# Optimization experiments

Measured on AMD Instinct MI355X. Metric: run time of the kernel, lower is better.

The kernel has to match this reference:

```python
import jax, jax.numpy as jnp
import numpy as np

D_MODEL, N_HEAD, D_HEAD = 1024, 16, 64
BATCH, Q_LEN = 2, 2048
LN_EPS = 1e-5


def _rel_shift(x):
    # x: [b, q, k, n] -- standard Transformer-XL relative shift
    b, q, k, n = x.shape
    zero_pad = jnp.zeros((b, q, 1, n), dtype=x.dtype)
    x_padded = jnp.concatenate([zero_pad, x], axis=2)      # [b, q, k+1, n]
    x_padded = x_padded.reshape(b, k + 1, q, n)
    return x_padded[:, 1:].reshape(b, q, k, n)


def _layer_norm(x, gamma, beta):
    mu = jnp.mean(x, axis=-1, keepdims=True)
    var = jnp.mean(jnp.square(x - mu), axis=-1, keepdims=True)
    return (x - mu) * jax.lax.rsqrt(var + LN_EPS) * gamma + beta


def setup_inputs() -> dict:
    key = jax.random.key(0)
    ks = jax.random.split(key, 8)
    inp = {
        "x": jax.random.normal(ks[0], (BATCH, Q_LEN, D_MODEL), jnp.float32),
        "relative_pos": jax.random.normal(ks[1], (Q_LEN, D_MODEL), jnp.float32),
        "r_w_bias": jax.random.normal(ks[2], (N_HEAD, D_HEAD), jnp.float32) * 0.02,
        "r_r_bias": jax.random.normal(ks[3], (N_HEAD, D_HEAD), jnp.float32) * 0.02,
        "attn_mask": jax.random.randint(ks[4], (BATCH, Q_LEN), 0, 2).astype(bool),
        "W_qkv": jax.random.normal(ks[5], (D_MODEL, 3 * N_HEAD * D_HEAD), jnp.float32) / np.sqrt(D_MODEL),
        "W_rel": jax.random.normal(ks[6], (D_MODEL, N_HEAD * D_HEAD), jnp.float32) / np.sqrt(D_MODEL),
        "W_out": jax.random.normal(ks[7], (N_HEAD * D_HEAD, D_MODEL), jnp.float32) / np.sqrt(N_HEAD * D_HEAD),
        "ln_gamma": jnp.ones((D_MODEL,), jnp.float32),
        "ln_beta": jnp.zeros((D_MODEL,), jnp.float32),
    }
    return inp


def reference(x, relative_pos, r_w_bias, r_r_bias, attn_mask, W_qkv, W_rel, W_out, ln_gamma, ln_beta):
    b, q_len, _ = x.shape
    r_len = relative_pos.shape[0]
    scale = 1.0 / np.sqrt(D_HEAD)

    w_heads = x @ W_qkv                                    # [b, q, 3*n*d]
    w_q, w_k, w_v = jnp.split(w_heads, 3, axis=-1)
    k_len = w_k.shape[1]

    w_q = w_q.reshape(b, q_len, N_HEAD, D_HEAD)
    w_k = w_k.reshape(b, k_len, N_HEAD, D_HEAD)
    w_v = w_v.reshape(b, k_len, N_HEAD, D_HEAD)
    r_k = (relative_pos @ W_rel).reshape(r_len, N_HEAD, D_HEAD)

    rw_q = w_q + r_w_bias                                  # [b, q, n, d]
    rr_q = w_q + r_r_bias

    ac = jnp.einsum('bind,bjnd->bijn', rw_q, w_k)          # content score
    bd = jnp.einsum('bind,jnd->bijn', rr_q, r_k)           # position score
    bd = _rel_shift(bd)

    attn_score = (ac + bd) * scale                         # [b, q, k, n]
    attn_score = jnp.where(attn_mask[:, None, :, None], -jnp.inf, attn_score)
    attn_prob = jax.nn.softmax(attn_score, axis=2)

    context = jnp.einsum('bijn,bjnd->bind', attn_prob, w_v)
    context = context.reshape(b, q_len, N_HEAD * D_HEAD)
    attn_out = context @ W_out
    return _layer_norm(x + attn_out, ln_gamma, ln_beta)
```

## Files before the change

### kernel.cpp

```cpp
#include <hip/hip_runtime.h>
#include <hip/hip_bf16.h>
#include <math.h>

#define S_LEN 2048
#define NHEAD 16
#define DHEAD 64
#define DMODEL 1024
#define NBATCH 2

typedef unsigned short u16;
typedef __attribute__((ext_vector_type(8))) short bf16x8;
typedef __attribute__((ext_vector_type(4))) short short4v;
typedef __attribute__((ext_vector_type(4))) float f32x4;

__device__ __forceinline__ short f2bs(float x) {
    __hip_bfloat16 h = __float2bfloat16(x);
    return __builtin_bit_cast(short, h);
}

#define GL2LDS(g, l)                                                         \
    __builtin_amdgcn_global_load_lds(                                        \
        (const __attribute__((address_space(1))) void*)(g),                  \
        (__attribute__((address_space(3))) void*)(l), 16, 0, 0)

__global__ __launch_bounds__(256) void cast_all(const float* __restrict__ x,
                                                const float* __restrict__ rpos,
                                                u16* __restrict__ xb,
                                                u16* __restrict__ rposb) {
    int bid = blockIdx.x;
    const float* in;
    u16* out;
    if (bid < 4096) { in = x; out = xb; }
    else            { in = rpos; out = rposb; bid -= 4096; }
    const int i = (bid * 256 + threadIdx.x) * 4;
    float4 v = *(const float4*)(in + i);
    short4v t;
    t[0] = f2bs(v.x); t[1] = f2bs(v.y); t[2] = f2bs(v.z); t[3] = f2bs(v.w);
    *(short4v*)(out + i) = t;
}

__global__ __launch_bounds__(256) void transp_cast_all(
    const float* __restrict__ Wqkv, const float* __restrict__ Wrel,
    const float* __restrict__ Wout,
    u16* __restrict__ Wqkvt, u16* __restrict__ Wrelt, u16* __restrict__ Woutt)
{
    __shared__ float t[64][65];
    int bx = blockIdx.x;
    const float* W;
    u16* Wt;
    int N;
    if (bx < 48)      { W = Wqkv; Wt = Wqkvt; N = 3 * DMODEL; }
    else if (bx < 64) { W = Wrel; Wt = Wrelt; N = DMODEL; bx -= 48; }
    else              { W = Wout; Wt = Woutt; N = DMODEL; bx -= 64; }
    const int k0 = blockIdx.y * 64, n0 = bx * 64;
    const int r = threadIdx.x >> 4;
    const int c4 = (threadIdx.x & 15) * 4;
    #pragma unroll
    for (int it = 0; it < 4; ++it) {
        float4 v = *(const float4*)(W + (size_t)(k0 + it * 16 + r) * N + n0 + c4);
        t[c4 + 0][it * 16 + r] = v.x;
        t[c4 + 1][it * 16 + r] = v.y;
        t[c4 + 2][it * 16 + r] = v.z;
        t[c4 + 3][it * 16 + r] = v.w;
    }
    __syncthreads();
    #pragma unroll
    for (int it = 0; it < 4; ++it) {
        const int nn = it * 16 + r;
        short4v o;
        o[0] = f2bs(t[nn][c4 + 0]); o[1] = f2bs(t[nn][c4 + 1]);
        o[2] = f2bs(t[nn][c4 + 2]); o[3] = f2bs(t[nn][c4 + 3]);
        *(short4v*)(Wt + (size_t)(n0 + nn) * DMODEL + k0 + c4) = o;
    }
}

#define GEMM_BODY(Aptr, Btptr, Kdim)                                          \
    __shared__ u16 As[128 * 64];                                              \
    __shared__ u16 Bs[128 * 64];                                              \
    const int tid = threadIdx.x;                                              \
    const int lane = tid & 63;                                                \
    const int w = tid >> 6;                                                   \
    const int quad = lane >> 4, col = lane & 15;                              \
    const int bm = blockIdx.y * 128, bn = blockIdx.x * 128;                   \
    const int wm = (w >> 1) * 64, wn = (w & 1) * 64;                          \
    f32x4 acc[4][4];                                                          \
    _Pragma("unroll")                                                         \
    for (int mt = 0; mt < 4; ++mt)                                            \
        _Pragma("unroll")                                                     \
        for (int nt = 0; nt < 4; ++nt) acc[mt][nt] = (f32x4){0.f,0.f,0.f,0.f};\
    for (int k0 = 0; k0 < (Kdim); k0 += 64) {                                 \
        _Pragma("unroll")                                                     \
        for (int it = 0; it < 4; ++it) {                                      \
            const int cb = it * 256 + w * 64;                                 \
            const int c = cb + lane;                                          \
            const int r = c >> 3;                                             \
            const int o = ((c & 7) ^ (r & 7)) * 8;                            \
            GL2LDS((Aptr) + (size_t)(bm + r) * (Kdim) + k0 + o, As + (size_t)cb * 8); \
            GL2LDS((Btptr) + (size_t)(bn + r) * (Kdim) + k0 + o, Bs + (size_t)cb * 8);\
        }                                                                     \
        __syncthreads();                                                      \
        _Pragma("unroll")                                                     \
        for (int kc = 0; kc < 2; ++kc) {                                      \
            bf16x8 af[4], bfr[4];                                             \
            _Pragma("unroll")                                                 \
            for (int t = 0; t < 4; ++t) {                                     \
                const int am = wm + t * 16 + col;                             \
                const int aj = kc * 4 + quad;                                 \
                af[t] = *(const bf16x8*)&As[(size_t)am * 64 + ((aj ^ (am & 7)) * 8)]; \
                const int bn2 = wn + t * 16 + col;                            \
                bfr[t] = *(const bf16x8*)&Bs[(size_t)bn2 * 64 + ((aj ^ (bn2 & 7)) * 8)]; \
            }                                                                 \
            _Pragma("unroll")                                                 \
            for (int mt = 0; mt < 4; ++mt)                                    \
                _Pragma("unroll")                                             \
                for (int nt = 0; nt < 4; ++nt)                                \
                    acc[mt][nt] = __builtin_amdgcn_mfma_f32_16x16x32_bf16(    \
                        af[mt], bfr[nt], acc[mt][nt], 0, 0, 0);               \
        }                                                                     \
        __syncthreads();                                                      \
    }

__global__ __launch_bounds__(256, 2) void gemm_qkv(
    const u16* __restrict__ A, const u16* __restrict__ Bt,
    const float* __restrict__ rwb, const float* __restrict__ rrb,
    u16* __restrict__ qrw_b, u16* __restrict__ qrr_b,
    u16* __restrict__ kb, u16* __restrict__ vbT)
{
    GEMM_BODY(A, Bt, DMODEL)
    #pragma unroll
    for (int mt = 0; mt < 4; ++mt) {
        const int row0 = bm + wm + mt * 16 + quad * 4;
        const int b = row0 >> 11;
        const int s0 = row0 & 2047;
        #pragma unroll
        for (int nt = 0; nt < 4; ++nt) {
            const int cn = bn + wn + nt * 16 + col;
            const int sec = cn >> 10;
            const int cc = cn & 1023;
            const int h = cc >> 6, d = cc & 63;
            const int bh = b * NHEAD + h;
            if (sec == 0) {
                const float bw = rwb[cc], br = rrb[cc];
                #pragma unroll
                for (int r = 0; r < 4; ++r) {
                    const size_t o = ((size_t)bh * S_LEN + s0 + r) * 64 + d;
                    qrw_b[o] = (u16)f2bs(acc[mt][nt][r] + bw);
                    qrr_b[o] = (u16)f2bs(acc[mt][nt][r] + br);
                }
            } else if (sec == 1) {
                #pragma unroll
                for (int r = 0; r < 4; ++r)
                    kb[((size_t)bh * S_LEN + s0 + r) * 64 + d] =
                        (u16)f2bs(acc[mt][nt][r]);
            } else {
                short4v t;
                t[0] = f2bs(acc[mt][nt][0]); t[1] = f2bs(acc[mt][nt][1]);
                t[2] = f2bs(acc[mt][nt][2]); t[3] = f2bs(acc[mt][nt][3]);
                *(short4v*)(vbT + ((size_t)bh * 64 + d) * S_LEN + s0) = t;
            }
        }
    }
}

__global__ __launch_bounds__(256, 2) void gemm_rel(
    const u16* __restrict__ A, const u16* __restrict__ Bt,
    u16* __restrict__ rkb)
{
    GEMM_BODY(A, Bt, DMODEL)
    #pragma unroll
    for (int mt = 0; mt < 4; ++mt) {
        const int l0 = bm + wm + mt * 16 + quad * 4;
        #pragma unroll
        for (int nt = 0; nt < 4; ++nt) {
            const int cn = bn + wn + nt * 16 + col;
            const int h = cn >> 6, d = cn & 63;
            #pragma unroll
            for (int r = 0; r < 4; ++r)
                rkb[((size_t)h * S_LEN + l0 + r) * 64 + d] =
                    (u16)f2bs(acc[mt][nt][r]);
        }
    }
}

__global__ __launch_bounds__(256, 2) void gemm_out(
    const u16* __restrict__ A, const u16* __restrict__ Bt,
    float* __restrict__ Cf, int N, int K)
{
    GEMM_BODY(A, Bt, K)
    #pragma unroll
    for (int mt = 0; mt < 4; ++mt)
        #pragma unroll
        for (int nt = 0; nt < 4; ++nt)
            #pragma unroll
            for (int r = 0; r < 4; ++r) {
                const int row = bm + wm + mt * 16 + quad * 4 + r;
                const int cn = bn + wn + nt * 16 + col;
                Cf[(size_t)row * N + cn] = acc[mt][nt][r];
            }
}

__global__ __launch_bounds__(512, 2) void flash_attn(
    const u16* __restrict__ qrw_b, const u16* __restrict__ qrr_b,
    const u16* __restrict__ kb, const u16* __restrict__ vbT,
    const u16* __restrict__ rkb, const int* __restrict__ mask,
    u16* __restrict__ ctxb)
{
    const int lane = threadIdx.x & 63;
    const int w    = threadIdx.x >> 6;
    const int quad = lane >> 4;
    const int col  = lane & 15;
    const int bh   = blockIdx.y;
    const int b    = bh >> 4;
    const int n    = bh & 15;
    const int B0   = blockIdx.x * 128;
    const int iw0  = B0 + w * 16;

    __shared__ u16 Ks[64 * 64];
    __shared__ u16 Vs[64 * 64];
    __shared__ u16 Rs[192 * 64];
    __shared__ u16 Pr[8][16][72];
    __shared__ float madd[S_LEN];

    const size_t headQ = (size_t)bh * S_LEN * 64;
    const size_t headR = (size_t)n  * S_LEN * 64;

    for (int i = threadIdx.x; i < S_LEN; i += 512)
        madd[i] = mask[b * S_LEN + i] ? -16384.f : 0.f;

    bf16x8 a_rw[2], a_rr0[2], a_rr1[2];
    {
        const int r0 = iw0 + col;
        const int r1 = (r0 + 1 < S_LEN) ? (r0 + 1) : (S_LEN - 1);
        #pragma unroll
        for (int kc = 0; kc < 2; ++kc) {
            const int doff = kc * 32 + quad * 8;
            a_rw[kc]  = *(const bf16x8*)(qrw_b + headQ + (size_t)r0 * 64 + doff);
            a_rr0[kc] = *(const bf16x8*)(qrr_b + headQ + (size_t)r0 * 64 + doff);
            a_rr1[kc] = *(const bf16x8*)(qrr_b + headQ + (size_t)r1 * 64 + doff);
        }
    }

    f32x4 O[4];
    float l_acc[4] = {0.f, 0.f, 0.f, 0.f};
    #pragma unroll
    for (int dt = 0; dt < 4; ++dt) O[dt] = (f32x4){0.f, 0.f, 0.f, 0.f};

    const int swz  = ((lane & 7) ^ ((lane >> 3) & 7)) * 8;
    const int lrow = lane >> 3;
    const int csel = col & 7;
    int roff = 0;

    for (int u0 = 0; u0 < S_LEN; u0 += 64) {
        const int dblk = B0 - u0;
        const int dw = dblk + 16 * w;
        const bool mixed = (dw >= 0) && (dw <= 48);
        const bool full = (u0 == 0) || (dblk == -64);
        const int pbase = (dblk >= 0) ? (S_LEN - 128 - dblk) : (-dblk - 129);
        __syncthreads();
        if (full) {
            roff = 0;
            #pragma unroll
            for (int t = 0; t < 5; ++t) {
                const int idx = w * 5 + t;
                if (idx < 8) {
                    GL2LDS(kb + headQ + (size_t)(u0 + idx * 8 + lrow) * 64 + swz,
                           Ks + idx * 512);
                } else if (idx < 16) {
                    const int c = idx - 8;
                    GL2LDS(vbT + ((size_t)bh * 64 + c * 8 + lrow) * S_LEN + u0 + swz,
                           Vs + c * 512);
                } else {
                    const int c = idx - 16;
                    int rr = pbase + c * 8 + lrow;
                    rr = rr < 0 ? 0 : (rr > S_LEN - 1 ? S_LEN - 1 : rr);
                    GL2LDS(rkb + headR + (size_t)rr * 64 + swz, Rs + c * 512);
                }
            }
        } else {
            const int old_roff = roff;
            roff += 64; if (roff >= 192) roff -= 192;
            #pragma unroll
            for (int t = 0; t < 3; ++t) {
                const int idx = w * 3 + t;
                if (idx < 8) {
                    GL2LDS(kb + headQ + (size_t)(u0 + idx * 8 + lrow) * 64 + swz,
                           Ks + idx * 512);
                } else if (idx < 16) {
                    const int c = idx - 8;
                    GL2LDS(vbT + ((size_t)bh * 64 + c * 8 + lrow) * S_LEN + u0 + swz,
                           Vs + c * 512);
                } else {
                    const int c = idx - 16;
                    int rr = pbase + 128 + c * 8 + lrow;
                    rr = rr < 0 ? 0 : (rr > S_LEN - 1 ? S_LEN - 1 : rr);
                    GL2LDS(rkb + headR + (size_t)rr * 64 + swz,
                           Rs + (size_t)(old_roff + c * 8) * 64);
                }
            }
        }
        bf16x8 rf2[5][2];
        if (mixed) {
            #pragma unroll
            for (int g = 0; g < 5; ++g) {
                const int u = g * 16 + col;
                int row = (dblk >= 0) ? (u - dw - 17) : (S_LEN - 16 - dw + u);
                row = row < 0 ? 0 : (row > S_LEN - 1 ? S_LEN - 1 : row);
                const u16* rb = rkb + headR + (size_t)row * 64 + quad * 8;
                rf2[g][0] = *(const bf16x8*)(rb);
                rf2[g][1] = *(const bf16x8*)(rb + 32);
            }
        }
        __syncthreads();

        f32x4 sc[4];
        #pragma unroll
        for (int nt = 0; nt < 4; ++nt) {
            const int m = nt * 16 + col;
            bf16x8 k0 = *(const bf16x8*)&Ks[m * 64 + ((quad ^ csel) * 8)];
            bf16x8 k1 = *(const bf16x8*)&Ks[m * 64 + (((4 + quad) ^ csel) * 8)];
            f32x4 c = (f32x4){0.f, 0.f, 0.f, 0.f};
            c = __builtin_amdgcn_mfma_f32_16x16x32_bf16(a_rw[0], k0, c, 0, 0, 0);
            c = __builtin_amdgcn_mfma_f32_16x16x32_bf16(a_rw[1], k1, c, 0, 0, 0);
            sc[nt] = c;
        }

        f32x4 pnl[5], oth[5];
        {
            const bf16x8* aP = (dblk >= 0) ? a_rr0 : a_rr1;
            #pragma unroll
            for (int g = 0; g < 5; ++g) {
                const int m = g * 16 + col + 112 - 16 * w;
                int slot = m + roff; if (slot >= 192) slot -= 192;
                bf16x8 r0 = *(const bf16x8*)&Rs[slot * 64 + ((quad ^ csel) * 8)];
                bf16x8 r1 = *(const bf16x8*)&Rs[slot * 64 + (((4 + quad) ^ csel) * 8)];
                f32x4 c = (f32x4){0.f, 0.f, 0.f, 0.f};
                c = __builtin_amdgcn_mfma_f32_16x16x32_bf16(aP[0], r0, c, 0, 0, 0);
                c = __builtin_amdgcn_mfma_f32_16x16x32_bf16(aP[1], r1, c, 0, 0, 0);
                pnl[g] = c;
            }
        }
        #pragma unroll
        for (int g = 0; g < 5; ++g) oth[g] = (f32x4){0.f, 0.f, 0.f, 0.f};
        if (mixed) {
            const bf16x8* aV = (dblk >= 0) ? a_rr1 : a_rr0;
            #pragma unroll
            for (int g = 0; g < 5; ++g) {
                f32x4 c = (f32x4){0.f, 0.f, 0.f, 0.f};
                c = __builtin_amdgcn_mfma_f32_16x16x32_bf16(aV[0], rf2[g][0], c, 0, 0, 0);
                c = __builtin_amdgcn_mfma_f32_16x16x32_bf16(aV[1], rf2[g][1], c, 0, 0, 0);
                oth[g] = c;
            }
        }
        const int lim1 = 15 + dw;
        #pragma unroll
        for (int g = 0; g < 5; ++g) {
            const int u = g * 16 + col;
            #pragma unroll
            for (int r = 0; r < 4; ++r) {
                const float r1v = (dblk >= 0) ? pnl[g][r] : oth[g][r];
                const float r2v = (dblk >= 0) ? oth[g][r] : pnl[g][r];
                pnl[g][r] = (u <= lim1) ? r1v : ((u == lim1 + 1) ? 0.f : r2v);
            }
        }

        #pragma unroll
        for (int nt = 0; nt < 4; ++nt) {
            const float ma = madd[u0 + nt * 16 + col];
            #pragma unroll
            for (int r = 0; r < 4; ++r) {
                const int uo = col + 15 - quad * 4 - r;
                const int src = (quad << 4) | (uo & 15);
                float blo = __shfl(pnl[nt][r], src, 64);
                float bhi = __shfl(pnl[nt + 1][r], src, 64);
                float bd = (uo < 16) ? blo : bhi;
                float p = __expf(fmaf(sc[nt][r] + bd, 0.125f, ma));
                sc[nt][r] = p;
                l_acc[r] += p;
            }
        }

        #pragma unroll
        for (int nt = 0; nt < 4; ++nt)
            #pragma unroll
            for (int r = 0; r < 4; ++r)
                Pr[w][quad * 4 + r][nt * 16 + col] = (u16)f2bs(sc[nt][r]);
        bf16x8 pa[2];
        pa[0] = *(const bf16x8*)&Pr[w][col][quad * 8];
        pa[1] = *(const bf16x8*)&Pr[w][col][32 + quad * 8];

        #pragma unroll
        for (int dt = 0; dt < 4; ++dt) {
            const int m = dt * 16 + col;
            bf16x8 v0 = *(const bf16x8*)&Vs[m * 64 + ((quad ^ csel) * 8)];
            bf16x8 v1 = *(const bf16x8*)&Vs[m * 64 + (((4 + quad) ^ csel) * 8)];
            f32x4 c = O[dt];
            c = __builtin_amdgcn_mfma_f32_16x16x32_bf16(pa[0], v0, c, 0, 0, 0);
            c = __builtin_amdgcn_mfma_f32_16x16x32_bf16(pa[1], v1, c, 0, 0, 0);
            O[dt] = c;
        }
    }

    float inv[4];
    #pragma unroll
    for (int r = 0; r < 4; ++r) {
        float s = l_acc[r];
        #pragma unroll
        for (int off = 1; off < 16; off <<= 1)
            s += __shfl_xor(s, off, 64);
        inv[r] = 1.f / s;
    }
    #pragma unroll
    for (int dt = 0; dt < 4; ++dt)
        #pragma unroll
        for (int r = 0; r < 4; ++r) {
            const int i = iw0 + quad * 4 + r;
            ctxb[((size_t)b * S_LEN + i) * DMODEL + n * 64 + dt * 16 + col] =
                (u16)f2bs(O[dt][r] * inv[r]);
        }
}

__global__ __launch_bounds__(256) void ln_kernel(const float* __restrict__ x,
                                                 const float* __restrict__ ao,
                                                 const float* __restrict__ gamma,
                                                 const float* __restrict__ beta,
                                                 float* __restrict__ out) {
    const int r = blockIdx.x;
    const int tid = threadIdx.x;
    const size_t base = (size_t)r * DMODEL + tid * 4;
    float4 xv = *(const float4*)(x + base);
    float4 av = *(const float4*)(ao + base);
    float v0 = xv.x + av.x, v1 = xv.y + av.y, v2 = xv.z + av.z, v3 = xv.w + av.w;

    float s = v0 + v1 + v2 + v3;
    #pragma unroll
    for (int off = 32; off > 0; off >>= 1) s += __shfl_xor(s, off, 64);
    __shared__ float red[4];
    __shared__ float red2[4];
    if ((tid & 63) == 0) red[tid >> 6] = s;
    __syncthreads();
    float mu = (red[0] + red[1] + red[2] + red[3]) * (1.0f / DMODEL);

    float d0 = v0 - mu, d1 = v1 - mu, d2 = v2 - mu, d3 = v3 - mu;
    float q = d0 * d0 + d1 * d1 + d2 * d2 + d3 * d3;
    #pragma unroll
    for (int off = 32; off > 0; off >>= 1) q += __shfl_xor(q, off, 64);
    if ((tid & 63) == 0) red2[tid >> 6] = q;
    __syncthreads();
    float var = (red2[0] + red2[1] + red2[2] + red2[3]) * (1.0f / DMODEL);
    float rstd = rsqrtf(var + 1e-5f);

    float4 g  = *(const float4*)(gamma + tid * 4);
    float4 be = *(const float4*)(beta + tid * 4);
    float4 o = make_float4(d0 * rstd * g.x + be.x,
                           d1 * rstd * g.y + be.y,
                           d2 * rstd * g.z + be.z,
                           d3 * rstd * g.w + be.w);
    *(float4*)(out + base) = o;
}

extern "C" void kernel_launch(void* const* d_in, const int* in_sizes, int n_in,
                              void* d_out, int out_size, void* d_ws, size_t ws_size,
                              hipStream_t stream) {
    const float* x    = (const float*)d_in[0];
    const float* rpos = (const float*)d_in[1];
    const float* rwb  = (const float*)d_in[2];
    const float* rrb  = (const float*)d_in[3];
    const int*   mask = (const int*)  d_in[4];
    const float* Wqkv = (const float*)d_in[5];
    const float* Wrel = (const float*)d_in[6];
    const float* Wout = (const float*)d_in[7];
    const float* gam  = (const float*)d_in[8];
    const float* bet  = (const float*)d_in[9];
    float* out = (float*)d_out;

    u16* wsb   = (u16*)d_ws;
    u16* ctxb  = wsb;
    float* ao  = (float*)(wsb + 4194304);
    u16* qrw_b = wsb + 12582912;
    u16* qrr_b = qrw_b + 4194304;
    u16* kb    = qrr_b + 4194304;
    u16* vbT   = kb + 4194304;
    u16* rkb   = vbT + 4194304;
    u16* xb    = rkb + 2097152;
    u16* rposb = xb + 4194304;
    u16* Wqkvt = rposb + 2097152;
    u16* Wrelt = Wqkvt + 3145728;
    u16* Woutt = Wrelt + 1048576;

    dim3 blk(256);
    cast_all<<<dim3(6144), blk, 0, stream>>>(x, rpos, xb, rposb);
    transp_cast_all<<<dim3(80, 16), blk, 0, stream>>>(Wqkv, Wrel, Wout,
                                                      Wqkvt, Wrelt, Woutt);
    gemm_qkv<<<dim3(24, 32), blk, 0, stream>>>(xb, Wqkvt, rwb, rrb,
                                               qrw_b, qrr_b, kb, vbT);
    gemm_rel<<<dim3(8, 16), blk, 0, stream>>>(rposb, Wrelt, rkb);
    flash_attn<<<dim3(S_LEN / 128, NBATCH * NHEAD), dim3(512), 0, stream>>>(
        qrw_b, qrr_b, kb, vbT, rkb, mask, ctxb);
    gemm_out<<<dim3(8, 32), blk, 0, stream>>>(ctxb, Woutt, ao, DMODEL, DMODEL);
    ln_kernel<<<dim3(NBATCH * S_LEN), blk, 0, stream>>>(x, ao, gam, bet, out);
}
```

Measured before the change: 351.7 us.

## Double-buffer K/V tiles and prefetch next relative-position rows in flash attention

Restructures the attention loop so the next K and V tiles are issued into a second LDS buffer while the current tile is computed. The next R rows are loaded into registers and written to the ring buffer after the P·V step. The goal is to hide global-load latency that was previously exposed behind the per-iteration barrier. It also stores the mask bias as bf16 and raises the launch-bounds occupancy hint from 2 to 4 blocks. That hint may cap registers severely and cause spills, while the larger LDS footprint may still limit residency.

```diff
diff --git a/kernel.cpp b/kernel.cpp
--- a/kernel.cpp
+++ b/kernel.cpp
@@ -16,6 +16,11 @@
 __device__ __forceinline__ short f2bs(float x) {
     __hip_bfloat16 h = __float2bfloat16(x);
     return __builtin_bit_cast(short, h);
+}
+
+__device__ __forceinline__ float bs2f(u16 x) {
+    __hip_bfloat16 h = __builtin_bit_cast(__hip_bfloat16, (short)x);
+    return __bfloat162float(h);
 }
 
 #define GL2LDS(g, l)                                                         \
@@ -199,7 +204,7 @@
             }
 }
 
-__global__ __launch_bounds__(512, 2) void flash_attn(
+__global__ __launch_bounds__(512, 4) void flash_attn(
     const u16* __restrict__ qrw_b, const u16* __restrict__ qrr_b,
     const u16* __restrict__ kb, const u16* __restrict__ vbT,
     const u16* __restrict__ rkb, const int* __restrict__ mask,
@@ -215,17 +220,17 @@
     const int B0   = blockIdx.x * 128;
     const int iw0  = B0 + w * 16;
 
-    __shared__ u16 Ks[64 * 64];
-    __shared__ u16 Vs[64 * 64];
+    __shared__ u16 Ks[2][64 * 64];
+    __shared__ u16 Vs[2][64 * 64];
     __shared__ u16 Rs[192 * 64];
     __shared__ u16 Pr[8][16][72];
-    __shared__ float madd[S_LEN];
+    __shared__ u16 maddb[S_LEN];
 
     const size_t headQ = (size_t)bh * S_LEN * 64;
     const size_t headR = (size_t)n  * S_LEN * 64;
 
     for (int i = threadIdx.x; i < S_LEN; i += 512)
-        madd[i] = mask[b * S_LEN + i] ? -16384.f : 0.f;
+        maddb[i] = (u16)f2bs(mask[b * S_LEN + i] ? -16384.f : 0.f);
 
     bf16x8 a_rw[2], a_rr0[2], a_rr1[2];
     {
@@ -248,56 +253,31 @@
     const int swz  = ((lane & 7) ^ ((lane >> 3) & 7)) * 8;
     const int lrow = lane >> 3;
     const int csel = col & 7;
+
+    {
+        const int pbase0 = S_LEN - 128 - B0;
+        GL2LDS(kb + headQ + (size_t)(w * 8 + lrow) * 64 + swz, Ks[0] + w * 512);
+        GL2LDS(vbT + ((size_t)bh * 64 + w * 8 + lrow) * S_LEN + swz, Vs[0] + w * 512);
+        #pragma unroll
+        for (int t = 0; t < 3; ++t) {
+            const int c = w * 3 + t;
+            int rr = pbase0 + c * 8 + lrow;
+            rr = rr < 0 ? 0 : (rr > S_LEN - 1 ? S_LEN - 1 : rr);
+            GL2LDS(rkb + headR + (size_t)rr * 64 + swz, Rs + c * 512);
+        }
+    }
     int roff = 0;
+    __syncthreads();
 
     for (int u0 = 0; u0 < S_LEN; u0 += 64) {
         const int dblk = B0 - u0;
         const int dw = dblk + 16 * w;
         const bool mixed = (dw >= 0) && (dw <= 48);
-        const bool full = (u0 == 0) || (dblk == -64);
-        const int pbase = (dblk >= 0) ? (S_LEN - 128 - dblk) : (-dblk - 129);
-        __syncthreads();
-        if (full) {
-            roff = 0;
-            #pragma unroll
-            for (int t = 0; t < 5; ++t) {
-                const int idx = w * 5 + t;
-                if (idx < 8) {
-                    GL2LDS(kb + headQ + (size_t)(u0 + idx * 8 + lrow) * 64 + swz,
-                           Ks + idx * 512);
-                } else if (idx < 16) {
-                    const int c = idx - 8;
-                    GL2LDS(vbT + ((size_t)bh * 64 + c * 8 + lrow) * S_LEN + u0 + swz,
-                           Vs + c * 512);
-                } else {
-                    const int c = idx - 16;
-                    int rr = pbase + c * 8 + lrow;
-                    rr = rr < 0 ? 0 : (rr > S_LEN - 1 ? S_LEN - 1 : rr);
-                    GL2LDS(rkb + headR + (size_t)rr * 64 + swz, Rs + c * 512);
-                }
-            }
-        } else {
-            const int old_roff = roff;
-            roff += 64; if (roff >= 192) roff -= 192;
-            #pragma unroll
-            for (int t = 0; t < 3; ++t) {
-                const int idx = w * 3 + t;
-                if (idx < 8) {
-                    GL2LDS(kb + headQ + (size_t)(u0 + idx * 8 + lrow) * 64 + swz,
-                           Ks + idx * 512);
-                } else if (idx < 16) {
-                    const int c = idx - 8;
-                    GL2LDS(vbT + ((size_t)bh * 64 + c * 8 + lrow) * S_LEN + u0 + swz,
-                           Vs + c * 512);
-                } else {
-                    const int c = idx - 16;
-                    int rr = pbase + 128 + c * 8 + lrow;
-                    rr = rr < 0 ? 0 : (rr > S_LEN - 1 ? S_LEN - 1 : rr);
-                    GL2LDS(rkb + headR + (size_t)rr * 64 + swz,
-                           Rs + (size_t)(old_roff + c * 8) * 64);
-                }
-            }
-        }
+        const int buf = (u0 >> 6) & 1;
+        const int u1 = u0 + 64;
+        const bool have_next = u1 < S_LEN;
+        const bool next_full = (B0 - u1) == -64;
+
         bf16x8 rf2[5][2];
         if (mixed) {
             #pragma unroll
@@ -310,14 +290,28 @@
                 rf2[g][1] = *(const bf16x8*)(rb + 32);
             }
         }
-        __syncthreads();
+
+        bf16x8 rpre;
+        if (have_next) {
+            GL2LDS(kb + headQ + (size_t)(u1 + w * 8 + lrow) * 64 + swz,
+                   Ks[buf ^ 1] + w * 512);
+            GL2LDS(vbT + ((size_t)bh * 64 + w * 8 + lrow) * S_LEN + u1 + swz,
+                   Vs[buf ^ 1] + w * 512);
+            if (!next_full) {
+                const int dn = B0 - u1;
+                const int pb = (dn >= 0) ? (S_LEN - 128 - dn) : (-dn - 129);
+                int rr = pb + 128 + w * 8 + lrow;
+                rr = rr < 0 ? 0 : (rr > S_LEN - 1 ? S_LEN - 1 : rr);
+                rpre = *(const bf16x8*)(rkb + headR + (size_t)rr * 64 + swz);
+            }
+        }
 
         f32x4 sc[4];
         #pragma unroll
         for (int nt = 0; nt < 4; ++nt) {
             const int m = nt * 16 + col;
-            bf16x8 k0 = *(const bf16x8*)&Ks[m * 64 + ((quad ^ csel) * 8)];
-            bf16x8 k1 = *(const bf16x8*)&Ks[m * 64 + (((4 + quad) ^ csel) * 8)];
+            bf16x8 k0 = *(const bf16x8*)&Ks[buf][m * 64 + ((quad ^ csel) * 8)];
+            bf16x8 k1 = *(const bf16x8*)&Ks[buf][m * 64 + (((4 + quad) ^ csel) * 8)];
             f32x4 c = (f32x4){0.f, 0.f, 0.f, 0.f};
             c = __builtin_amdgcn_mfma_f32_16x16x32_bf16(a_rw[0], k0, c, 0, 0, 0);
             c = __builtin_amdgcn_mfma_f32_16x16x32_bf16(a_rw[1], k1, c, 0, 0, 0);
@@ -365,7 +359,7 @@
 
         #pragma unroll
         for (int nt = 0; nt < 4; ++nt) {
-            const float ma = madd[u0 + nt * 16 + col];
+            const float ma = bs2f(maddb[u0 + nt * 16 + col]);
             #pragma unroll
             for (int r = 0; r < 4; ++r) {
                 const int uo = col + 15 - quad * 4 - r;
@@ -391,12 +385,30 @@
         #pragma unroll
         for (int dt = 0; dt < 4; ++dt) {
             const int m = dt * 16 + col;
-            bf16x8 v0 = *(const bf16x8*)&Vs[m * 64 + ((quad ^ csel) * 8)];
-            bf16x8 v1 = *(const bf16x8*)&Vs[m * 64 + (((4 + quad) ^ csel) * 8)];
+            bf16x8 v0 = *(const bf16x8*)&Vs[buf][m * 64 + ((quad ^ csel) * 8)];
+            bf16x8 v1 = *(const bf16x8*)&Vs[buf][m * 64 + (((4 + quad) ^ csel) * 8)];
             f32x4 c = O[dt];
             c = __builtin_amdgcn_mfma_f32_16x16x32_bf16(pa[0], v0, c, 0, 0, 0);
             c = __builtin_amdgcn_mfma_f32_16x16x32_bf16(pa[1], v1, c, 0, 0, 0);
             O[dt] = c;
+        }
+
+        if (have_next) {
+            __syncthreads();
+            if (next_full) {
+                #pragma unroll
+                for (int t = 0; t < 3; ++t) {
+                    const int c = w * 3 + t;
+                    int rr = -65 + c * 8 + lrow;
+                    rr = rr < 0 ? 0 : (rr > S_LEN - 1 ? S_LEN - 1 : rr);
+                    GL2LDS(rkb + headR + (size_t)rr * 64 + swz, Rs + c * 512);
+                }
+                roff = 0;
+            } else {
+                *(bf16x8*)&Rs[((size_t)(roff + w * 8) << 6) + lane * 8] = rpre;
+                roff += 64; if (roff >= 192) roff -= 192;
+            }
+            __syncthreads();
         }
     }
 
```

After: 397.9 us. 13.2% more time.
